# Optimization experiments

Measured on AMD Instinct MI355X. Metric: run time of the kernel, lower is better.

The kernel has to match this reference:

```python
import jax, jax.numpy as jnp
import numpy as np

C = 256
HEADS = 8
DIM = C // HEADS
SCALE = DIM ** -0.5


def setup_inputs() -> dict:
    key = jax.random.key(0)
    ks = jax.random.split(key, 6)
    B, T, H, W = 2, 8, 128, 128
    x = jax.random.normal(ks[0], (B, T, C, H, W), dtype=jnp.float32)
    relativeBias = jax.random.normal(ks[1], (HEADS, H, H), dtype=jnp.float32)
    # nn.Linear params (PyTorch convention: y = x @ W.T + b)
    w_qkv = jax.random.normal(ks[2], (3 * C, C), dtype=jnp.float32) * (C ** -0.5)
    b_qkv = jax.random.normal(ks[3], (3 * C,), dtype=jnp.float32) * 0.02
    w_proj = jax.random.normal(ks[4], (C, C), dtype=jnp.float32) * (C ** -0.5)
    b_proj = jax.random.normal(ks[5], (C,), dtype=jnp.float32) * 0.02
    return {"x": x, "relativeBias": relativeBias, "w_qkv": w_qkv,
            "b_qkv": b_qkv, "w_proj": w_proj, "b_proj": b_proj}


def reference(x, relativeBias, w_qkv, b_qkv, w_proj, b_proj):
    B, T, Cc, H, W = x.shape
    # axis == 'height': fold (B,T,W) into line dim, attend along H
    seq = jnp.transpose(x, (0, 1, 4, 3, 2)).reshape(B * T * W, H, Cc)  # (N,L,C)
    qkv = seq @ w_qkv.T + b_qkv                                        # (N,L,3C)
    q, k, v = jnp.split(qkv, 3, axis=-1)
    N, L = seq.shape[0], seq.shape[1]
    q = q.reshape(N, L, HEADS, DIM)
    k = k.reshape(N, L, HEADS, DIM)
    v = v.reshape(N, L, HEADS, DIM)
    attn = jnp.einsum('nlhd,nmhd->nhlm', q, k) * SCALE + relativeBias  # (N,h,L,L)
    attn = jax.nn.softmax(attn, axis=-1)
    o = jnp.einsum('nhlm,nmhd->nlhd', attn, v).reshape(N, L, Cc)
    out = o @ w_proj.T + b_proj                                        # (N,L,C)
    # invert: (B,T,W,H,C) -> (B,T,C,H,W)
    return jnp.transpose(out.reshape(B, T, W, H, Cc), (0, 1, 4, 3, 2))
```

## Files before the change

kernel.cpp:

```cpp
#include <hip/hip_runtime.h>

#define B_ 2
#define T_ 8
#define C_ 256
#define H_ 128
#define W_ 128
#define NBT (B_*T_)
#define L_ 128
#define HEADS_ 8
#define DIM_ 32
#define C3 (3*C_)
#define SCALE_ 0.17677669529663687f
#define LOG2E_ 1.4426950408889634f

typedef __bf16 bf16x8 __attribute__((ext_vector_type(8)));
typedef float f32x4 __attribute__((ext_vector_type(4)));
typedef unsigned short ush;
typedef unsigned short u16x4 __attribute__((ext_vector_type(4)));
typedef unsigned int uint_a __attribute__((may_alias));

__device__ __forceinline__ ush f2bf(float f){
  union { float f; unsigned int u; } v; v.f = f;
  unsigned int r = v.u + 0x7fffu + ((v.u >> 16) & 1u);
  return (ush)(r >> 16);
}

#if __has_builtin(__builtin_amdgcn_exp2f)
#define EXP2(x) __builtin_amdgcn_exp2f(x)
#else
#define EXP2(x) exp2f(x)
#endif

#if __has_builtin(__builtin_amdgcn_global_load_lds)
#define HAVE_GLL 1
typedef __attribute__((address_space(3))) ush lds_ush;
typedef __attribute__((address_space(1))) const ush glb_ush;
__device__ __forceinline__ void gll16(const ush* g, ush* l){
  __builtin_amdgcn_global_load_lds((glb_ush*)g, (lds_ush*)l, 16, 0, 0);
}
#endif

__global__ __launch_bounds__(256) void k_setup(const float* __restrict__ wq, const float* __restrict__ wp,
                                               const float* __restrict__ rb,
                                               ush* __restrict__ wqb, ush* __restrict__ wpb,
                                               float* __restrict__ be){
  int i = blockIdx.x*256 + threadIdx.x;
  if (i < C3*C_) wqb[i] = f2bf(wq[i]);
  if (i < C_*C_) wpb[i] = f2bf(wp[i]);
  if (i < HEADS_*L_*L_){
    int col = i & (L_-1);
    int hrow = i >> 7;
    int tgt = ((hrow<<4) + (col & 15))*8 + (col >> 4);
    be[tgt] = rb[i]*LOG2E_;
  }
}

__global__ __launch_bounds__(256) void k_trans(const float* __restrict__ x, ush* __restrict__ xT, int bt0){
  __shared__ float tile[64*129];
  const int l   = blockIdx.x & (L_-1);
  const int btL = blockIdx.x >> 7;
  const int t = threadIdx.x;
  const float* xp = x + (size_t)(bt0 + btL)*C_*H_*W_ + (size_t)l*W_;
  ush* xo = xT + ((size_t)blockIdx.x) * W_ * C_;
  const int wI = t & (W_-1);
  const int chh = t >> 7;
  const int c2 = (t & 31)*2;
  const int wr0 = t >> 5;
  for (int cs = 0; cs < 4; ++cs){
    #pragma unroll 4
    for (int i = 0; i < 32; ++i){
      int cl = chh*32 + i;
      tile[cl*129 + wI] = xp[(size_t)(cs*64 + cl)*(H_*W_) + wI];
    }
    __syncthreads();
    #pragma unroll 4
    for (int i = 0; i < 16; ++i){
      int wr = wr0 + i*8;
      float v0 = tile[c2*129 + wr];
      float v1 = tile[(c2+1)*129 + wr];
      unsigned int pk = (unsigned int)f2bf(v0) | ((unsigned int)f2bf(v1) << 16);
      *(uint_a*)(xo + (size_t)wr*C_ + cs*64 + c2) = pk;
    }
    __syncthreads();
  }
}

__global__ __launch_bounds__(256) void k_qkv(const ush* __restrict__ xT, const ush* __restrict__ wqb,
                                             const float* __restrict__ bq, ush* __restrict__ qkv,
                                             int nbtl){
  int idx = blockIdx.x;
  int lo3 = idx & 7, rest = idx >> 3;
  int nt = rest % 6, hi = rest / 6;
  int btl = hi*8 + lo3;
  const int l = btl & (L_-1), btL = btl >> 7;
  const int oc0 = nt*128;
  __shared__ ush lA[2*128*64];
  __shared__ ush lB[2*128*64];
  const int t = threadIdx.x;
  const int lane = t & 63, wv = t >> 6;
  const int wm = (wv >> 1)*64, wn = (wv & 1)*64;
  const int li = lane & 15, g = lane >> 4;
  f32x4 acc[4][4] = {};
  const ush* aBase = xT + (size_t)btl * W_ * C_;
  const ush* bBase = wqb + (size_t)oc0 * C_;
  const int rowOff = lane >> 3;
  const int srcCl  = (lane & 7) ^ rowOff;
  auto stage = [&](int buf, int ks){
#ifdef HAVE_GLL
    #pragma unroll
    for (int c = 0; c < 4; ++c){
      int chunk = wv*4 + c;
      int row = chunk*8 + rowOff;
      gll16(aBase + (size_t)row*C_ + ks*64 + srcCl*8, &lA[buf*8192 + chunk*512]);
      gll16(bBase + (size_t)row*C_ + ks*64 + srcCl*8, &lB[buf*8192 + chunk*512]);
    }
#else
    #pragma unroll
    for (int j = 0; j < 4; ++j){
      int cid = j*256 + t;
      int row = cid >> 3, cl = cid & 7;
      int sw = ((cl ^ (row & 7)) << 3);
      *(bf16x8*)&lA[buf*8192 + row*64 + sw] = *(const bf16x8*)&aBase[(size_t)row*C_ + ks*64 + cl*8];
      *(bf16x8*)&lB[buf*8192 + row*64 + sw] = *(const bf16x8*)&bBase[(size_t)row*C_ + ks*64 + cl*8];
    }
#endif
  };
  stage(0, 0);
  __syncthreads();
  int cur = 0;
  for (int ks = 0; ks < 4; ++ks){
    if (ks < 3) stage(cur^1, ks+1);
    #pragma unroll
    for (int kk = 0; kk < 2; ++kk){
      bf16x8 af[4], bfr[4];
      int chunk = kk*4 + g;
      #pragma unroll
      for (int mf = 0; mf < 4; ++mf){
        int row = wm + mf*16 + li;
        af[mf] = *(const bf16x8*)&lA[cur*8192 + row*64 + ((chunk ^ (row & 7)) << 3)];
      }
      #pragma unroll
      for (int nf = 0; nf < 4; ++nf){
        int row = wn + nf*16 + li;
        bfr[nf] = *(const bf16x8*)&lB[cur*8192 + row*64 + ((chunk ^ (row & 7)) << 3)];
      }
      #pragma unroll
      for (int mf = 0; mf < 4; ++mf)
        #pragma unroll
        for (int nf = 0; nf < 4; ++nf)
          acc[mf][nf] = __builtin_amdgcn_mfma_f32_16x16x32_bf16(af[mf], bfr[nf], acc[mf][nf], 0, 0, 0);
    }
    __syncthreads();
    cur ^= 1;
  }
  float bqv[4];
  #pragma unroll
  for (int nf = 0; nf < 4; ++nf) bqv[nf] = bq[oc0 + wn + nf*16 + li];
  #pragma unroll
  for (int mf = 0; mf < 4; ++mf){
    #pragma unroll
    for (int r = 0; r < 4; ++r){
      int w = wm + mf*16 + 4*g + r;
      size_t base = (((size_t)btL*W_ + w)*L_ + l)*C3 + oc0;
      #pragma unroll
      for (int nf = 0; nf < 4; ++nf){
        qkv[base + wn + nf*16 + li] = f2bf(acc[mf][nf][r] + bqv[nf]);
      }
    }
  }
}

__global__ __launch_bounds__(64) void k_attn(const ush* __restrict__ qkv, const float* __restrict__ biasE,
                                             ush* __restrict__ o){
  int idx = blockIdx.x;
  int lo3 = idx & 7, rest = idx >> 3;
  int h = rest & 7;
  int ln = (rest >> 3)*8 + lo3;
  const ush* qkvL = qkv + (size_t)ln * L_ * C3;
  ush* oL = o + (size_t)ln * L_ * C_;
  __shared__ ush sbuf[32*136];
  const int lane = threadIdx.x;
  const int li = lane & 15, g = lane >> 4;
  const float KS = SCALE_ * LOG2E_;
  bf16x8 kb[8];
  #pragma unroll
  for (int nf = 0; nf < 8; ++nf){
    int key = nf*16 + li;
    kb[nf] = *(const bf16x8*)&qkvL[(size_t)key*C3 + C_ + h*DIM_ + 8*g];
  }
  {
    int key8 = lane >> 3, d4 = (lane & 7)*4;
    for (int it = 0; it < 16; ++it){
      int key = it*8 + key8;
      u16x4 vv = *(const u16x4*)&qkvL[(size_t)key*C3 + 2*C_ + h*DIM_ + d4];
      #pragma unroll
      for (int j = 0; j < 4; ++j) sbuf[(d4 + j)*136 + key] = vv[j];
    }
  }
  __syncthreads();
  bf16x8 vb[2][4];
  #pragma unroll
  for (int nf = 0; nf < 2; ++nf)
    #pragma unroll
    for (int kk = 0; kk < 4; ++kk)
      vb[nf][kk] = *(const bf16x8*)&sbuf[(nf*16 + li)*136 + kk*32 + 8*g];
  __syncthreads();
  const float* bh = biasE + (size_t)h * L_ * L_;
  for (int rbk = 0; rbk < 4; ++rbk){
    bf16x8 qa[2];
    #pragma unroll
    for (int mf = 0; mf < 2; ++mf){
      int q = rbk*32 + mf*16 + li;
      qa[mf] = *(const bf16x8*)&qkvL[(size_t)q*C3 + h*DIM_ + 8*g];
    }
    f32x4 s[2][8] = {};
    __builtin_amdgcn_s_setprio(1);
    #pragma unroll
    for (int mf = 0; mf < 2; ++mf)
      #pragma unroll
      for (int nf = 0; nf < 8; ++nf)
        s[mf][nf] = __builtin_amdgcn_mfma_f32_16x16x32_bf16(qa[mf], kb[nf], s[mf][nf], 0, 0, 0);
    __builtin_amdgcn_s_setprio(0);
    float rrs[2][4];
    #pragma unroll
    for (int mf = 0; mf < 2; ++mf)
      #pragma unroll
      for (int r = 0; r < 4; ++r){
        int row = rbk*32 + mf*16 + 4*g + r;
        const f32x4* bp2 = (const f32x4*)&bh[((size_t)row*16 + li)*8];
        f32x4 b0 = bp2[0], b1 = bp2[1];
        float sum = 0.f;
        #pragma unroll
        for (int nf = 0; nf < 8; ++nf){
          float bb = (nf < 4) ? b0[nf] : b1[nf & 3];
          float e = EXP2(s[mf][nf][r]*KS + bb);
          s[mf][nf][r] = e;
          sum += e;
        }
        #pragma unroll
        for (int d = 1; d < 16; d <<= 1) sum += __shfl_xor(sum, d, 64);
        rrs[mf][r] = 1.0f / sum;
      }
    #pragma unroll
    for (int mf = 0; mf < 2; ++mf)
      #pragma unroll
      for (int r = 0; r < 4; ++r){
        int rl = mf*16 + 4*g + r;
        #pragma unroll
        for (int nf = 0; nf < 8; ++nf)
          sbuf[rl*136 + nf*16 + li] = f2bf(s[mf][nf][r]);
      }
    __syncthreads();
    f32x4 oacc[2][2] = {};
    #pragma unroll
    for (int kk = 0; kk < 4; ++kk){
      bf16x8 pa[2];
      #pragma unroll
      for (int mf = 0; mf < 2; ++mf)
        pa[mf] = *(const bf16x8*)&sbuf[(mf*16 + li)*136 + kk*32 + 8*g];
      __builtin_amdgcn_s_setprio(1);
      #pragma unroll
      for (int mf = 0; mf < 2; ++mf)
        #pragma unroll
        for (int nf = 0; nf < 2; ++nf)
          oacc[mf][nf] = __builtin_amdgcn_mfma_f32_16x16x32_bf16(pa[mf], vb[nf][kk], oacc[mf][nf], 0, 0, 0);
      __builtin_amdgcn_s_setprio(0);
    }
    #pragma unroll
    for (int mf = 0; mf < 2; ++mf)
      #pragma unroll
      for (int r = 0; r < 4; ++r){
        int q = rbk*32 + mf*16 + 4*g + r;
        #pragma unroll
        for (int nf = 0; nf < 2; ++nf)
          oL[(size_t)q*C_ + h*DIM_ + nf*16 + li] = f2bf(oacc[mf][nf][r] * rrs[mf][r]);
      }
    __syncthreads();
  }
}

__global__ __launch_bounds__(256) void k_proj(const ush* __restrict__ oIn, const ush* __restrict__ wpb,
                                              const float* __restrict__ bp, float* __restrict__ out,
                                              int nbtl, int bt0){
  int idx = blockIdx.x;
  int lo3 = idx & 7, rest = idx >> 3;
  int mt = rest & 1, hi = rest >> 1;
  int btl = hi*8 + lo3;
  const int l = btl & (L_-1), btL = btl >> 7;
  __shared__ ush lA[2*128*64];
  __shared__ ush lB[2*128*64];
  const int t = threadIdx.x;
  const int lane = t & 63, wv = t >> 6;
  const int wm = (wv >> 1)*64, wn = (wv & 1)*64;
  const int li = lane & 15, g = lane >> 4;
  f32x4 acc[4][4] = {};
  const ush* aBase = wpb + (size_t)mt*128*C_;
  const ush* bBase = oIn + ((size_t)btL*W_*L_ + l)*C_;
  const int rowOff = lane >> 3;
  const int srcCl  = (lane & 7) ^ rowOff;
  auto stage = [&](int buf, int ks){
#ifdef HAVE_GLL
    #pragma unroll
    for (int c = 0; c < 4; ++c){
      int chunk = wv*4 + c;
      int row = chunk*8 + rowOff;
      gll16(aBase + (size_t)row*C_        + ks*64 + srcCl*8, &lA[buf*8192 + chunk*512]);
      gll16(bBase + (size_t)row*(L_*C_)   + ks*64 + srcCl*8, &lB[buf*8192 + chunk*512]);
    }
#else
    #pragma unroll
    for (int j = 0; j < 4; ++j){
      int cid = j*256 + t;
      int row = cid >> 3, cl = cid & 7;
      int sw = ((cl ^ (row & 7)) << 3);
      *(bf16x8*)&lA[buf*8192 + row*64 + sw] = *(const bf16x8*)&aBase[(size_t)row*C_ + ks*64 + cl*8];
      *(bf16x8*)&lB[buf*8192 + row*64 + sw] = *(const bf16x8*)&bBase[(size_t)row*(L_*C_) + ks*64 + cl*8];
    }
#endif
  };
  stage(0, 0);
  __syncthreads();
  int cur = 0;
  for (int ks = 0; ks < 4; ++ks){
    if (ks < 3) stage(cur^1, ks+1);
    #pragma unroll
    for (int kk = 0; kk < 2; ++kk){
      bf16x8 af[4], bfr[4];
      int chunk = kk*4 + g;
      #pragma unroll
      for (int mf = 0; mf < 4; ++mf){
        int row = wm + mf*16 + li;
        af[mf] = *(const bf16x8*)&lA[cur*8192 + row*64 + ((chunk ^ (row & 7)) << 3)];
      }
      #pragma unroll
      for (int nf = 0; nf < 4; ++nf){
        int row = wn + nf*16 + li;
        bfr[nf] = *(const bf16x8*)&lB[cur*8192 + row*64 + ((chunk ^ (row & 7)) << 3)];
      }
      #pragma unroll
      for (int mf = 0; mf < 4; ++mf)
        #pragma unroll
        for (int nf = 0; nf < 4; ++nf)
          acc[mf][nf] = __builtin_amdgcn_mfma_f32_16x16x32_bf16(af[mf], bfr[nf], acc[mf][nf], 0, 0, 0);
    }
    __syncthreads();
    cur ^= 1;
  }
  #pragma unroll
  for (int mf = 0; mf < 4; ++mf){
    #pragma unroll
    for (int r = 0; r < 4; ++r){
      int c = mt*128 + wm + mf*16 + 4*g + r;
      float bias = bp[c];
      size_t rowbase = (((size_t)(bt0 + btL)*C_ + c)*H_ + l)*W_;
      #pragma unroll
      for (int nf = 0; nf < 4; ++nf){
        out[rowbase + wn + nf*16 + li] = acc[mf][nf][r] + bias;
      }
    }
  }
}

extern "C" void kernel_launch(void* const* d_in, const int* in_sizes, int n_in,
                              void* d_out, int out_size, void* d_ws, size_t ws_size,
                              hipStream_t stream){
  const float* x  = (const float*)d_in[0];
  const float* rb = (const float*)d_in[1];
  const float* wq = (const float*)d_in[2];
  const float* bq = (const float*)d_in[3];
  const float* wp = (const float*)d_in[4];
  const float* bp = (const float*)d_in[5];
  float* out = (float*)d_out;
  char* ws = (char*)d_ws;
  ush* wqb = (ush*)ws;
  ush* wpb = wqb + C3*C_;
  size_t wend = ((size_t)(C3*C_ + C_*C_)*2 + 255) & ~(size_t)255;
  float* biasE = (float*)(ws + wend);
  size_t base = (wend + (size_t)HEADS_*L_*L_*4 + 255) & ~(size_t)255;
  const size_t xT_bt  = (size_t)L_*W_*C_*2;
  const size_t qkv_bt = (size_t)W_*L_*C3*2;
  const size_t o_bt   = (size_t)W_*L_*C_*2;
  const size_t per_bt = xT_bt + qkv_bt + o_bt;
  int G = (ws_size > base) ? (int)((ws_size - base) / per_bt) : 0;
  if (G > NBT) G = NBT;
  if (G > 4)   G = 4;
  if (G < 1)   G = 1;

  k_setup<<<dim3((C3*C_ + 255)/256), dim3(256), 0, stream>>>(wq, wp, rb, wqb, wpb, biasE);

  for (int bt0 = 0; bt0 < NBT; bt0 += G){
    int gc = (NBT - bt0 < G) ? (NBT - bt0) : G;
    ush* xT  = (ush*)(ws + base);
    ush* qkv = (ush*)(ws + base + (size_t)gc*xT_bt);
    ush* oB  = (ush*)(ws + base + (size_t)gc*(xT_bt + qkv_bt));
    int nbtl = gc*L_;
    k_trans<<<dim3(nbtl),    dim3(256), 0, stream>>>(x, xT, bt0);
    k_qkv  <<<dim3(6*nbtl),  dim3(256), 0, stream>>>(xT, wqb, bq, qkv, nbtl);
    k_attn <<<dim3(8*gc*W_), dim3(64),  0, stream>>>(qkv, biasE, oB);
    k_proj <<<dim3(2*nbtl),  dim3(256), 0, stream>>>(oB, wpb, bp, out, nbtl, bt0);
  }
}
```

Baseline: 503.2 us.

## Fuse QKV projection into attention kernel per line and head

Merges the QKV GEMM and the attention kernel into one kernel. Each block computes the Q, K and V slices for one line and one head in shared memory, then runs attention on them directly. This removes the global round-trip of the bf16 qkv intermediate and one kernel launch per group. In exchange the x tile for a line is re-read once per head, and the block uses a larger shared-memory footprint that may limit occupancy.

```diff
diff --git a/kernel.cpp b/kernel.cpp
--- a/kernel.cpp
+++ b/kernel.cpp
@@ -12,6 +12,7 @@
 #define C3 (3*C_)
 #define SCALE_ 0.17677669529663687f
 #define LOG2E_ 1.4426950408889634f
+#define QSTR 104
 
 typedef __bf16 bf16x8 __attribute__((ext_vector_type(8)));
 typedef float f32x4 __attribute__((ext_vector_type(4)));
@@ -85,34 +86,40 @@
   }
 }
 
-__global__ __launch_bounds__(256) void k_qkv(const ush* __restrict__ xT, const ush* __restrict__ wqb,
-                                             const float* __restrict__ bq, ush* __restrict__ qkv,
-                                             int nbtl){
+__global__ __launch_bounds__(256) void k_qkvattn(const ush* __restrict__ xT, const ush* __restrict__ wqb,
+                                                 const float* __restrict__ bq, const float* __restrict__ biasE,
+                                                 ush* __restrict__ o){
+  __shared__ ush smem[30720];
   int idx = blockIdx.x;
   int lo3 = idx & 7, rest = idx >> 3;
-  int nt = rest % 6, hi = rest / 6;
-  int btl = hi*8 + lo3;
-  const int l = btl & (L_-1), btL = btl >> 7;
-  const int oc0 = nt*128;
-  __shared__ ush lA[2*128*64];
-  __shared__ ush lB[2*128*64];
+  int h = rest & 7;
+  int lw = (rest >> 3)*8 + lo3;
+  const int btL = lw >> 7, w = lw & (W_-1);
   const int t = threadIdx.x;
   const int lane = t & 63, wv = t >> 6;
-  const int wm = (wv >> 1)*64, wn = (wv & 1)*64;
   const int li = lane & 15, g = lane >> 4;
-  f32x4 acc[4][4] = {};
-  const ush* aBase = xT + (size_t)btl * W_ * C_;
-  const ush* bBase = wqb + (size_t)oc0 * C_;
+  ush* lA = smem;
+  ush* lB = smem + 16384;
+  ush* qkvt = smem;
+  ush* pTw = smem + 128*QSTR + wv*(32*136);
+  const ush* xA = xT + (size_t)btL*L_*W_*C_ + (size_t)w*C_;
   const int rowOff = lane >> 3;
   const int srcCl  = (lane & 7) ^ rowOff;
+  f32x4 acc[2][6] = {};
   auto stage = [&](int buf, int ks){
 #ifdef HAVE_GLL
     #pragma unroll
     for (int c = 0; c < 4; ++c){
       int chunk = wv*4 + c;
       int row = chunk*8 + rowOff;
-      gll16(aBase + (size_t)row*C_ + ks*64 + srcCl*8, &lA[buf*8192 + chunk*512]);
-      gll16(bBase + (size_t)row*C_ + ks*64 + srcCl*8, &lB[buf*8192 + chunk*512]);
+      gll16(xA + (size_t)row*(W_*C_) + ks*64 + srcCl*8, &lA[buf*8192 + chunk*512]);
+    }
+    #pragma unroll
+    for (int c = 0; c < 3; ++c){
+      int chunk = wv*3 + c;
+      int row = chunk*8 + rowOff;
+      int wr = (row >> 5)*C_ + h*DIM_ + (row & 31);
+      gll16(wqb + (size_t)wr*C_ + ks*64 + srcCl*8, &lB[buf*6144 + chunk*512]);
     }
 #else
     #pragma unroll
@@ -120,8 +127,17 @@
       int cid = j*256 + t;
       int row = cid >> 3, cl = cid & 7;
       int sw = ((cl ^ (row & 7)) << 3);
-      *(bf16x8*)&lA[buf*8192 + row*64 + sw] = *(const bf16x8*)&aBase[(size_t)row*C_ + ks*64 + cl*8];
-      *(bf16x8*)&lB[buf*8192 + row*64 + sw] = *(const bf16x8*)&bBase[(size_t)row*C_ + ks*64 + cl*8];
+      *(bf16x8*)&lA[buf*8192 + row*64 + sw] = *(const bf16x8*)&xA[(size_t)row*(W_*C_) + ks*64 + cl*8];
+    }
+    #pragma unroll
+    for (int j = 0; j < 3; ++j){
+      int cid = j*256 + t;
+      int row = cid >> 3, cl = cid & 7;
+      if (row < 96){
+        int wr = (row >> 5)*C_ + h*DIM_ + (row & 31);
+        int sw = ((cl ^ (row & 7)) << 3);
+        *(bf16x8*)&lB[buf*6144 + row*64 + sw] = *(const bf16x8*)&wqb[(size_t)wr*C_ + ks*64 + cl*8];
+      }
     }
 #endif
   };
@@ -132,151 +148,127 @@
     if (ks < 3) stage(cur^1, ks+1);
     #pragma unroll
     for (int kk = 0; kk < 2; ++kk){
-      bf16x8 af[4], bfr[4];
+      bf16x8 af[2], bfr[6];
       int chunk = kk*4 + g;
       #pragma unroll
-      for (int mf = 0; mf < 4; ++mf){
-        int row = wm + mf*16 + li;
+      for (int mf = 0; mf < 2; ++mf){
+        int row = wv*32 + mf*16 + li;
         af[mf] = *(const bf16x8*)&lA[cur*8192 + row*64 + ((chunk ^ (row & 7)) << 3)];
       }
       #pragma unroll
-      for (int nf = 0; nf < 4; ++nf){
-        int row = wn + nf*16 + li;
-        bfr[nf] = *(const bf16x8*)&lB[cur*8192 + row*64 + ((chunk ^ (row & 7)) << 3)];
-      }
-      #pragma unroll
-      for (int mf = 0; mf < 4; ++mf)
+      for (int nf = 0; nf < 6; ++nf){
+        int row = nf*16 + li;
+        bfr[nf] = *(const bf16x8*)&lB[cur*6144 + row*64 + ((chunk ^ (row & 7)) << 3)];
+      }
+      #pragma unroll
+      for (int mf = 0; mf < 2; ++mf)
         #pragma unroll
-        for (int nf = 0; nf < 4; ++nf)
+        for (int nf = 0; nf < 6; ++nf)
           acc[mf][nf] = __builtin_amdgcn_mfma_f32_16x16x32_bf16(af[mf], bfr[nf], acc[mf][nf], 0, 0, 0);
     }
     __syncthreads();
     cur ^= 1;
   }
-  float bqv[4];
-  #pragma unroll
-  for (int nf = 0; nf < 4; ++nf) bqv[nf] = bq[oc0 + wn + nf*16 + li];
-  #pragma unroll
-  for (int mf = 0; mf < 4; ++mf){
-    #pragma unroll
-    for (int r = 0; r < 4; ++r){
-      int w = wm + mf*16 + 4*g + r;
-      size_t base = (((size_t)btL*W_ + w)*L_ + l)*C3 + oc0;
-      #pragma unroll
-      for (int nf = 0; nf < 4; ++nf){
-        qkv[base + wn + nf*16 + li] = f2bf(acc[mf][nf][r] + bqv[nf]);
-      }
-    }
-  }
-}
-
-__global__ __launch_bounds__(64) void k_attn(const ush* __restrict__ qkv, const float* __restrict__ biasE,
-                                             ush* __restrict__ o){
-  int idx = blockIdx.x;
-  int lo3 = idx & 7, rest = idx >> 3;
-  int h = rest & 7;
-  int ln = (rest >> 3)*8 + lo3;
-  const ush* qkvL = qkv + (size_t)ln * L_ * C3;
-  ush* oL = o + (size_t)ln * L_ * C_;
-  __shared__ ush sbuf[32*136];
-  const int lane = threadIdx.x;
-  const int li = lane & 15, g = lane >> 4;
+  float bqv[6];
+  #pragma unroll
+  for (int nf = 0; nf < 6; ++nf){
+    int col = nf*16 + li;
+    bqv[nf] = bq[(col >> 5)*C_ + h*DIM_ + (col & 31)];
+  }
+  #pragma unroll
+  for (int mf = 0; mf < 2; ++mf)
+    #pragma unroll
+    for (int r = 0; r < 4; ++r){
+      int m = wv*32 + mf*16 + 4*g + r;
+      #pragma unroll
+      for (int nf = 0; nf < 6; ++nf)
+        qkvt[m*QSTR + nf*16 + li] = f2bf(acc[mf][nf][r] + bqv[nf]);
+    }
+  __syncthreads();
   const float KS = SCALE_ * LOG2E_;
   bf16x8 kb[8];
   #pragma unroll
-  for (int nf = 0; nf < 8; ++nf){
-    int key = nf*16 + li;
-    kb[nf] = *(const bf16x8*)&qkvL[(size_t)key*C3 + C_ + h*DIM_ + 8*g];
-  }
-  {
-    int key8 = lane >> 3, d4 = (lane & 7)*4;
-    for (int it = 0; it < 16; ++it){
-      int key = it*8 + key8;
-      u16x4 vv = *(const u16x4*)&qkvL[(size_t)key*C3 + 2*C_ + h*DIM_ + d4];
-      #pragma unroll
-      for (int j = 0; j < 4; ++j) sbuf[(d4 + j)*136 + key] = vv[j];
-    }
-  }
+  for (int nf = 0; nf < 8; ++nf)
+    kb[nf] = *(const bf16x8*)&qkvt[(nf*16 + li)*QSTR + DIM_ + 8*g];
+  bf16x8 vb[2][4];
+  #pragma unroll
+  for (int nf = 0; nf < 2; ++nf)
+    #pragma unroll
+    for (int kk = 0; kk < 4; ++kk){
+      ush tmp[8];
+      #pragma unroll
+      for (int j = 0; j < 8; ++j)
+        tmp[j] = qkvt[(kk*32 + 8*g + j)*QSTR + 2*DIM_ + nf*16 + li];
+      __builtin_memcpy(&vb[nf][kk], tmp, 16);
+    }
+  bf16x8 qa[2];
+  #pragma unroll
+  for (int mf = 0; mf < 2; ++mf)
+    qa[mf] = *(const bf16x8*)&qkvt[(wv*32 + mf*16 + li)*QSTR + 8*g];
+  const float* bh = biasE + (size_t)h * L_ * L_;
+  f32x4 s[2][8] = {};
+  __builtin_amdgcn_s_setprio(1);
+  #pragma unroll
+  for (int mf = 0; mf < 2; ++mf)
+    #pragma unroll
+    for (int nf = 0; nf < 8; ++nf)
+      s[mf][nf] = __builtin_amdgcn_mfma_f32_16x16x32_bf16(qa[mf], kb[nf], s[mf][nf], 0, 0, 0);
+  __builtin_amdgcn_s_setprio(0);
+  float rrs[2][4];
+  #pragma unroll
+  for (int mf = 0; mf < 2; ++mf)
+    #pragma unroll
+    for (int r = 0; r < 4; ++r){
+      int row = wv*32 + mf*16 + 4*g + r;
+      const f32x4* bp2 = (const f32x4*)&bh[((size_t)row*16 + li)*8];
+      f32x4 b0 = bp2[0], b1 = bp2[1];
+      float sum = 0.f;
+      #pragma unroll
+      for (int nf = 0; nf < 8; ++nf){
+        float bb = (nf < 4) ? b0[nf] : b1[nf & 3];
+        float e = EXP2(s[mf][nf][r]*KS + bb);
+        s[mf][nf][r] = e;
+        sum += e;
+      }
+      #pragma unroll
+      for (int d = 1; d < 16; d <<= 1) sum += __shfl_xor(sum, d, 64);
+      rrs[mf][r] = 1.0f / sum;
+    }
+  #pragma unroll
+  for (int mf = 0; mf < 2; ++mf)
+    #pragma unroll
+    for (int r = 0; r < 4; ++r){
+      int rl = mf*16 + 4*g + r;
+      #pragma unroll
+      for (int nf = 0; nf < 8; ++nf)
+        pTw[rl*136 + nf*16 + li] = f2bf(s[mf][nf][r]);
+    }
   __syncthreads();
-  bf16x8 vb[2][4];
-  #pragma unroll
-  for (int nf = 0; nf < 2; ++nf)
-    #pragma unroll
-    for (int kk = 0; kk < 4; ++kk)
-      vb[nf][kk] = *(const bf16x8*)&sbuf[(nf*16 + li)*136 + kk*32 + 8*g];
-  __syncthreads();
-  const float* bh = biasE + (size_t)h * L_ * L_;
-  for (int rbk = 0; rbk < 4; ++rbk){
-    bf16x8 qa[2];
-    #pragma unroll
-    for (int mf = 0; mf < 2; ++mf){
-      int q = rbk*32 + mf*16 + li;
-      qa[mf] = *(const bf16x8*)&qkvL[(size_t)q*C3 + h*DIM_ + 8*g];
-    }
-    f32x4 s[2][8] = {};
+  f32x4 oacc[2][2] = {};
+  #pragma unroll
+  for (int kk = 0; kk < 4; ++kk){
+    bf16x8 pa[2];
+    #pragma unroll
+    for (int mf = 0; mf < 2; ++mf)
+      pa[mf] = *(const bf16x8*)&pTw[(mf*16 + li)*136 + kk*32 + 8*g];
     __builtin_amdgcn_s_setprio(1);
     #pragma unroll
     for (int mf = 0; mf < 2; ++mf)
       #pragma unroll
-      for (int nf = 0; nf < 8; ++nf)
-        s[mf][nf] = __builtin_amdgcn_mfma_f32_16x16x32_bf16(qa[mf], kb[nf], s[mf][nf], 0, 0, 0);
+      for (int nf = 0; nf < 2; ++nf)
+        oacc[mf][nf] = __builtin_amdgcn_mfma_f32_16x16x32_bf16(pa[mf], vb[nf][kk], oacc[mf][nf], 0, 0, 0);
     __builtin_amdgcn_s_setprio(0);
-    float rrs[2][4];
-    #pragma unroll
-    for (int mf = 0; mf < 2; ++mf)
-      #pragma unroll
-      for (int r = 0; r < 4; ++r){
-        int row = rbk*32 + mf*16 + 4*g + r;
-        const f32x4* bp2 = (const f32x4*)&bh[((size_t)row*16 + li)*8];
-        f32x4 b0 = bp2[0], b1 = bp2[1];
-        float sum = 0.f;
-        #pragma unroll
-        for (int nf = 0; nf < 8; ++nf){
-          float bb = (nf < 4) ? b0[nf] : b1[nf & 3];
-          float e = EXP2(s[mf][nf][r]*KS + bb);
-          s[mf][nf][r] = e;
-          sum += e;
-        }
-        #pragma unroll
-        for (int d = 1; d < 16; d <<= 1) sum += __shfl_xor(sum, d, 64);
-        rrs[mf][r] = 1.0f / sum;
-      }
-    #pragma unroll
-    for (int mf = 0; mf < 2; ++mf)
-      #pragma unroll
-      for (int r = 0; r < 4; ++r){
-        int rl = mf*16 + 4*g + r;
-        #pragma unroll
-        for (int nf = 0; nf < 8; ++nf)
-          sbuf[rl*136 + nf*16 + li] = f2bf(s[mf][nf][r]);
-      }
-    __syncthreads();
-    f32x4 oacc[2][2] = {};
-    #pragma unroll
-    for (int kk = 0; kk < 4; ++kk){
-      bf16x8 pa[2];
-      #pragma unroll
-      for (int mf = 0; mf < 2; ++mf)
-        pa[mf] = *(const bf16x8*)&sbuf[(mf*16 + li)*136 + kk*32 + 8*g];
-      __builtin_amdgcn_s_setprio(1);
-      #pragma unroll
-      for (int mf = 0; mf < 2; ++mf)
-        #pragma unroll
-        for (int nf = 0; nf < 2; ++nf)
-          oacc[mf][nf] = __builtin_amdgcn_mfma_f32_16x16x32_bf16(pa[mf], vb[nf][kk], oacc[mf][nf], 0, 0, 0);
-      __builtin_amdgcn_s_setprio(0);
-    }
-    #pragma unroll
-    for (int mf = 0; mf < 2; ++mf)
-      #pragma unroll
-      for (int r = 0; r < 4; ++r){
-        int q = rbk*32 + mf*16 + 4*g + r;
-        #pragma unroll
-        for (int nf = 0; nf < 2; ++nf)
-          oL[(size_t)q*C_ + h*DIM_ + nf*16 + li] = f2bf(oacc[mf][nf][r] * rrs[mf][r]);
-      }
-    __syncthreads();
-  }
+  }
+  ush* oL = o + (size_t)lw * L_ * C_;
+  #pragma unroll
+  for (int mf = 0; mf < 2; ++mf)
+    #pragma unroll
+    for (int r = 0; r < 4; ++r){
+      int q = wv*32 + mf*16 + 4*g + r;
+      #pragma unroll
+      for (int nf = 0; nf < 2; ++nf)
+        oL[(size_t)q*C_ + h*DIM_ + nf*16 + li] = f2bf(oacc[mf][nf][r] * rrs[mf][r]);
+    }
 }
 
 __global__ __launch_bounds__(256) void k_proj(const ush* __restrict__ oIn, const ush* __restrict__ wpb,
@@ -378,9 +370,8 @@
   float* biasE = (float*)(ws + wend);
   size_t base = (wend + (size_t)HEADS_*L_*L_*4 + 255) & ~(size_t)255;
   const size_t xT_bt  = (size_t)L_*W_*C_*2;
-  const size_t qkv_bt = (size_t)W_*L_*C3*2;
   const size_t o_bt   = (size_t)W_*L_*C_*2;
-  const size_t per_bt = xT_bt + qkv_bt + o_bt;
+  const size_t per_bt = xT_bt + o_bt;
   int G = (ws_size > base) ? (int)((ws_size - base) / per_bt) : 0;
   if (G > NBT) G = NBT;
   if (G > 4)   G = 4;
@@ -391,12 +382,10 @@
   for (int bt0 = 0; bt0 < NBT; bt0 += G){
     int gc = (NBT - bt0 < G) ? (NBT - bt0) : G;
     ush* xT  = (ush*)(ws + base);
-    ush* qkv = (ush*)(ws + base + (size_t)gc*xT_bt);
-    ush* oB  = (ush*)(ws + base + (size_t)gc*(xT_bt + qkv_bt));
+    ush* oB  = (ush*)(ws + base + (size_t)gc*xT_bt);
     int nbtl = gc*L_;
-    k_trans<<<dim3(nbtl),    dim3(256), 0, stream>>>(x, xT, bt0);
-    k_qkv  <<<dim3(6*nbtl),  dim3(256), 0, stream>>>(xT, wqb, bq, qkv, nbtl);
-    k_attn <<<dim3(8*gc*W_), dim3(64),  0, stream>>>(qkv, biasE, oB);
-    k_proj <<<dim3(2*nbtl),  dim3(256), 0, stream>>>(oB, wpb, bp, out, nbtl, bt0);
-  }
-}
+    k_trans   <<<dim3(nbtl),      dim3(256), 0, stream>>>(x, xT, bt0);
+    k_qkvattn <<<dim3(8*gc*W_),   dim3(256), 0, stream>>>(xT, wqb, bq, biasE, oB);
+    k_proj    <<<dim3(2*nbtl),    dim3(256), 0, stream>>>(oB, wpb, bp, out, nbtl, bt0);
+  }
+}
```

Result: faster. 459.8 us (-8.6%).
